# Kernel optimization log

Hardware: AMD Instinct MI355X
Metric: run time of the kernel (lower is better)

The kernel has to match this reference:

```python
import jax, jax.numpy as jnp
import numpy as np

B, N, H, HEADS = 8, 1024, 512, 4  # batch graphs, nodes/graph, graph_hsz, attention heads
R = 64  # relations per graph (passthrough)


def setup_inputs() -> dict:
    key = jax.random.key(0)
    k1, k2, k3, k4, k5, k6, k7 = jax.random.split(key, 7)
    adjs = jax.random.randint(k1, (B, N, N), 0, 2, dtype=jnp.int32)  # 0 => masked
    nodes = jax.random.normal(k2, (B, N, H), dtype=jnp.float32)
    triples = jax.random.normal(k3, (B, R, H), dtype=jnp.float32)   # unused in gat path
    relations = jax.random.normal(k4, (B, R, H), dtype=jnp.float32)  # passthrough
    node_num = jnp.full((B,), N, dtype=jnp.int32)  # all graphs full => no padding branch
    s = 1.0 / np.sqrt(H)
    Wq = (jax.random.normal(k5, (H, H), dtype=jnp.float32) * s)
    Wk = (jax.random.normal(k6, (H, H), dtype=jnp.float32) * s)
    Wv = (jax.random.normal(k7, (H, H), dtype=jnp.float32) * s)
    return {"adjs": adjs, "triples": triples, "nodes": nodes, "node_num": node_num,
            "relations": relations, "Wq": Wq, "Wk": Wk, "Wv": Wv}


def reference(adjs, triples, nodes, node_num, relations, Wq, Wk, Wv):
    b, n, h = nodes.shape
    dk = h // HEADS
    scale = 1.0 / jnp.sqrt(jnp.float32(h))  # torch divides by sqrt(key_dim)=sqrt(H)

    def to_heads(x, W):  # [B,N,H] -> [B,heads,N,dk]; matches split(dim=-1)+stack
        return (x @ W).reshape(b, n, HEADS, dk).transpose(0, 2, 1, 3)

    Q = to_heads(nodes, Wq)
    K = to_heads(nodes, Wk)
    V = to_heads(nodes, Wv)
    att = jnp.einsum('bhnd,bhmd->bhnm', Q, K) * scale
    att = jnp.where((adjs == 0)[:, None, :, :], -jnp.inf, att)
    p = jax.nn.softmax(att, axis=-1)  # dropout_p = blockdrop = 0.0 => identity
    out = jnp.einsum('bhnm,bhmd->bhnd', p, V)
    out = out.transpose(0, 2, 1, 3).reshape(b, n, h)  # concat heads along feature dim
    out = jax.nn.relu(out)
    return (out, relations)
```

## Files before the change

### kernel.cpp

```cpp
#include <hip/hip_runtime.h>
#include <stdint.h>

typedef __attribute__((ext_vector_type(4))) float f32x4;
typedef __attribute__((ext_vector_type(16))) float f32x16;
typedef __attribute__((ext_vector_type(8))) short bf16x8;
typedef unsigned long long ull;

#define GLB_AS const __attribute__((address_space(1)))
#define LDS_AS __attribute__((address_space(3)))

__device__ __forceinline__ short f2bf(float f) {
    union { float f; unsigned u; } x; x.f = f;
    unsigned r = x.u + 0x7FFFu + ((x.u >> 16) & 1u);
    return (short)(r >> 16);
}
__device__ __forceinline__ float bf2f(short s) {
    union { unsigned u; float f; } x; x.u = ((unsigned)(unsigned short)s) << 16;
    return x.f;
}

__global__ void k_pre(const float* __restrict__ nodes, short* __restrict__ nodes_bf,
                      const float* __restrict__ Wq, const float* __restrict__ Wk,
                      const float* __restrict__ Wv, short* __restrict__ WT,
                      const int* __restrict__ adjs, unsigned* __restrict__ packed) {
    int bi = blockIdx.x, tid = threadIdx.x;
    if (bi < 2048) {
        int i = (bi * 256 + tid) * 8;
        float4 a = *(const float4*)(nodes + i);
        float4 b = *(const float4*)(nodes + i + 4);
        bf16x8 v;
        v[0] = f2bf(a.x); v[1] = f2bf(a.y); v[2] = f2bf(a.z); v[3] = f2bf(a.w);
        v[4] = f2bf(b.x); v[5] = f2bf(b.y); v[6] = f2bf(b.z); v[7] = f2bf(b.w);
        *(bf16x8*)(nodes_bf + i) = v;
    } else if (bi < 5120) {
        int g = (bi - 2048) * 256 + tid;
        int j = g >> 9, k = g & 511;
        int w = j >> 9, n = j & 511;
        const float* W = (w == 0) ? Wq : (w == 1) ? Wk : Wv;
        WT[g] = f2bf(W[k * 512 + n]);
    } else {
        int g = (bi - 5120) * 256 + tid;
        int wv = g >> 6, lane = g & 63;
        ull m = __ballot(adjs[(size_t)wv * 64 + lane] != 0);
        if (lane == 0) *(ull*)(packed + (size_t)wv * 2) = m;
    }
}

__global__ __launch_bounds__(256) void k_gemm_qkv(const short* __restrict__ A,
                                                  const short* __restrict__ WT,
                                                  short* __restrict__ C) {
    __shared__ short Asm[2][128 * 32];
    __shared__ short Bsm[2][128 * 32];
    const int tid = threadIdx.x;
    const int l = tid & 63, w = tid >> 6;
    const int wr = w >> 1, wc = w & 1;
    const int c16 = l & 15, g = l >> 4;
    const int wg = blockIdx.x;
    const int swz = (wg & 7) * 96 + (wg >> 3);
    const int row0 = (swz / 12) * 128, n0 = (swz % 12) * 128;
    f32x4 acc[4][4] = {};

    auto stage = [&](int kt, int bsel) {
        const int k0 = kt * 32;
#pragma unroll
        for (int i = 0; i < 2; ++i) {
            int ch = tid + 256 * i;
            int r = ch >> 2, gc = ch & 3;
            __builtin_amdgcn_global_load_lds((GLB_AS unsigned*)(A + (row0 + r) * 512 + k0 + 8 * gc),
                                             (LDS_AS unsigned*)(&Asm[bsel][ch * 8]), 16, 0, 0);
            __builtin_amdgcn_global_load_lds((GLB_AS unsigned*)(WT + (n0 + r) * 512 + k0 + 8 * gc),
                                             (LDS_AS unsigned*)(&Bsm[bsel][ch * 8]), 16, 0, 0);
        }
    };

    stage(0, 0);
    asm volatile("s_waitcnt vmcnt(0)" ::: "memory");
    __syncthreads();

    for (int kt = 0; kt < 16; ++kt) {
        const int cur = kt & 1;
        if (kt < 15) stage(kt + 1, cur ^ 1);
        bf16x8 af[4], bfr[4];
#pragma unroll
        for (int mf = 0; mf < 4; ++mf)
            af[mf] = *(const bf16x8*)&Asm[cur][(wr * 64 + mf * 16 + c16) * 32 + 8 * g];
#pragma unroll
        for (int nf = 0; nf < 4; ++nf)
            bfr[nf] = *(const bf16x8*)&Bsm[cur][(wc * 64 + nf * 16 + c16) * 32 + 8 * g];
#pragma unroll
        for (int mf = 0; mf < 4; ++mf)
#pragma unroll
            for (int nf = 0; nf < 4; ++nf)
                acc[mf][nf] = __builtin_amdgcn_mfma_f32_16x16x32_bf16(af[mf], bfr[nf], acc[mf][nf], 0, 0, 0);
        asm volatile("s_waitcnt vmcnt(0)" ::: "memory");
        __syncthreads();
    }
#pragma unroll
    for (int mf = 0; mf < 4; ++mf)
#pragma unroll
        for (int nf = 0; nf < 4; ++nf) {
            const float cs = (n0 + wc * 64 + nf * 16 < 512) ? 0.06375872022286384f : 1.0f;
#pragma unroll
            for (int r = 0; r < 4; ++r) {
                int row = row0 + wr * 64 + mf * 16 + 4 * g + r;
                int col = n0 + wc * 64 + nf * 16 + c16;
                C[row * 1536 + col] = f2bf(acc[mf][nf][r] * cs);
            }
        }
}

__global__ __launch_bounds__(256) void k_mid(const short* __restrict__ QKV, short* __restrict__ Vt,
                                             const float* __restrict__ rel_in, float* __restrict__ rel_out) {
    __shared__ short tile[64 * 65];
    const int bi = blockIdx.x, t = threadIdx.x;
    if (bi >= 1024) {
        int i = ((bi - 1024) * 256 + t) * 4;
        *(float4*)(rel_out + i) = *(const float4*)(rel_in + i);
        return;
    }
    const int b = bi >> 7, n0 = ((bi >> 3) & 15) * 64, d0 = (bi & 7) * 64;
#pragma unroll
    for (int i = 0; i < 16; ++i) {
        int idx = t + 256 * i;
        int nn = idx >> 6, dd = idx & 63;
        tile[nn * 65 + dd] = QKV[(b * 1024 + n0 + nn) * 1536 + 1024 + d0 + dd];
    }
    __syncthreads();
#pragma unroll
    for (int i = 0; i < 16; ++i) {
        int idx = t + 256 * i;
        int dd = idx >> 6, nn = idx & 63;
        Vt[(b * 512 + d0 + dd) * 1024 + n0 + nn] = tile[nn * 65 + dd];
    }
}

__global__ __launch_bounds__(256, 2) void k_attn(const short* __restrict__ QKV, const short* __restrict__ Vt,
                                                 const unsigned* __restrict__ packed,
                                                 float* __restrict__ o0, short* __restrict__ o1,
                                                 float* __restrict__ lpart) {
    __shared__ short Ksm[2][64 * 128];
    __shared__ short Vsm[2][128 * 64];
    const int bh = blockIdx.x;
    const int b = bh >> 2, h = bh & 3;
    const int q0 = blockIdx.y * 128;
    const int mh = blockIdx.z;
    const int tid = threadIdx.x, l = tid & 63, wid = tid >> 6;
    const int l31 = l & 31, hi = l >> 5;
    const int qw = q0 + wid * 32;
    const int mbase = mh * 512;

    bf16x8 aq[8];
    const short* Qb = QKV + (size_t)(b * 1024 + qw + l31) * 1536 + h * 128;
#pragma unroll
    for (int kk = 0; kk < 8; ++kk)
        aq[kk] = *(const bf16x8*)(Qb + kk * 16 + hi * 8);

    f32x16 acc[4] = {};
    float l_lane = 0.f;

    const short* Kbase = QKV + (size_t)(b * 1024) * 1536 + 512 + h * 128;
    const short* Vtbase = Vt + (size_t)(b * 512 + h * 128) * 1024;
    const ull* adjq = (const ull*)packed + (size_t)(b * 1024 + qw + l31) * 16 + mh * 8;

    auto stage = [&](int t, int bsel) {
        const int m0 = mbase + t * 64;
#pragma unroll
        for (int i = 0; i < 4; ++i) {
            int ch = tid + 256 * i;
            int mr = ch >> 4, gc = ch & 15;
            int gs = gc ^ (mr & 15);
            __builtin_amdgcn_global_load_lds((GLB_AS unsigned*)(Kbase + (size_t)(m0 + mr) * 1536 + 8 * gs),
                                             (LDS_AS unsigned*)(&Ksm[bsel][ch * 8]), 16, 0, 0);
        }
#pragma unroll
        for (int i = 0; i < 4; ++i) {
            int ch = tid + 256 * i;
            int dr = ch >> 3, gc = ch & 7;
            int gs = gc ^ (dr & 7);
            __builtin_amdgcn_global_load_lds((GLB_AS unsigned*)(Vtbase + (size_t)dr * 1024 + m0 + 8 * gs),
                                             (LDS_AS unsigned*)(&Vsm[bsel][ch * 8]), 16, 0, 0);
        }
    };

    ull mcur = adjq[0], mnxt = 0;
    stage(0, 0);
    asm volatile("s_waitcnt vmcnt(0)" ::: "memory");
    __builtin_amdgcn_s_barrier();

    for (int t = 0; t < 8; ++t) {
        const int cur = t & 1;
        if (t < 7) {
            mnxt = adjq[t + 1];
            stage(t + 1, cur ^ 1);
        }

        f32x16 s[2] = {};
        __builtin_amdgcn_s_setprio(1);
#pragma unroll
        for (int kk = 0; kk < 8; ++kk)
#pragma unroll
            for (int mm = 0; mm < 2; ++mm) {
                const int row = mm * 32 + l31;
                const int chunk = (2 * kk + hi) ^ (row & 15);
                bf16x8 ak = *(const bf16x8*)&Ksm[cur][row * 128 + chunk * 8];
                s[mm] = __builtin_amdgcn_mfma_f32_32x32x16_bf16(ak, aq[kk], s[mm], 0, 0, 0);
            }
        __builtin_amdgcn_s_setprio(0);

        unsigned pk[2][4][2];
        float lt = 0.f;
#pragma unroll
        for (int mm = 0; mm < 2; ++mm) {
            const unsigned mshift = (unsigned)(mcur >> (32 * mm + 4 * hi));
#pragma unroll
            for (int j = 0; j < 4; ++j) {
                float p[4];
#pragma unroll
                for (int r = 0; r < 4; ++r) {
                    float e = __builtin_amdgcn_exp2f(s[mm][4 * j + r]);
                    p[r] = ((mshift >> (8 * j + r)) & 1u) ? e : 0.f;
                }
                lt += (p[0] + p[1]) + (p[2] + p[3]);
                asm("v_cvt_pk_bf16_f32 %0, %1, %2" : "=v"(pk[mm][j][0]) : "v"(p[0]), "v"(p[1]));
                asm("v_cvt_pk_bf16_f32 %0, %1, %2" : "=v"(pk[mm][j][1]) : "v"(p[2]), "v"(p[3]));
            }
        }
        l_lane += lt;

        union fragu { unsigned u[4]; bf16x8 v; };
        fragu frag[4];
#pragma unroll
        for (int mm = 0; mm < 2; ++mm)
#pragma unroll
            for (int kh = 0; kh < 2; ++kh) {
                unsigned a0 = pk[mm][2 * kh][0], a1 = pk[mm][2 * kh][1];
                unsigned b0 = pk[mm][2 * kh + 1][0], b1 = pk[mm][2 * kh + 1][1];
                unsigned rx0 = (unsigned)__shfl_xor((int)a0, 32);
                unsigned rx1 = (unsigned)__shfl_xor((int)a1, 32);
                unsigned rx2 = (unsigned)__shfl_xor((int)b0, 32);
                unsigned rx3 = (unsigned)__shfl_xor((int)b1, 32);
                fragu f;
                f.u[0] = hi ? rx2 : a0;
                f.u[1] = hi ? rx3 : a1;
                f.u[2] = hi ? b0 : rx0;
                f.u[3] = hi ? b1 : rx1;
                frag[2 * mm + kh] = f;
            }

        if (t < 7) { asm volatile("s_waitcnt vmcnt(9)" ::: "memory"); }
        else       { asm volatile("s_waitcnt vmcnt(0)" ::: "memory"); }
        __builtin_amdgcn_s_barrier();

        __builtin_amdgcn_s_setprio(1);
#pragma unroll
        for (int ks = 0; ks < 4; ++ks)
#pragma unroll
            for (int dd = 0; dd < 4; ++dd) {
                const int row = dd * 32 + l31;
                const int chunk = (2 * ks + hi) ^ (row & 7);
                bf16x8 bv = *(const bf16x8*)&Vsm[cur][row * 64 + chunk * 8];
                acc[dd] = __builtin_amdgcn_mfma_f32_32x32x16_bf16(frag[ks].v, bv, acc[dd], 0, 0, 0);
            }
        __builtin_amdgcn_s_setprio(0);

        mcur = mnxt;

        if (t < 7) {
            asm volatile("s_waitcnt vmcnt(4)" ::: "memory");
            __builtin_amdgcn_s_barrier();
        }
    }

    l_lane += __shfl_xor(l_lane, 32);

    if (mh == 0) {
#pragma unroll
        for (int dd = 0; dd < 4; ++dd)
#pragma unroll
            for (int j = 0; j < 4; ++j)
#pragma unroll
                for (int r = 0; r < 4; ++r) {
                    int q32 = r + 8 * j + 4 * hi;
                    o0[(size_t)(b * 1024 + qw + q32) * 512 + h * 128 + dd * 32 + l31] = acc[dd][4 * j + r];
                }
    } else {
#pragma unroll
        for (int dd = 0; dd < 4; ++dd)
#pragma unroll
            for (int j = 0; j < 4; ++j)
#pragma unroll
                for (int r = 0; r < 4; ++r) {
                    int q32 = r + 8 * j + 4 * hi;
                    o1[(size_t)(b * 1024 + qw + q32) * 512 + h * 128 + dd * 32 + l31] = f2bf(acc[dd][4 * j + r]);
                }
    }
    if (hi == 0)
        lpart[mh * 32768 + (b * 4 + h) * 1024 + qw + l31] = l_lane;
}

__global__ void k_combine(float* __restrict__ out, const short* __restrict__ o1,
                          const float* __restrict__ lp) {
    int i = (blockIdx.x * 256 + threadIdx.x) * 8;
    int b = i >> 19;
    int q = (i >> 9) & 1023;
    int h = (i >> 7) & 3;
    int lidx = (b * 4 + h) * 1024 + q;
    float inv = 1.f / (lp[lidx] + lp[32768 + lidx]);
    float4 a0 = *(const float4*)(out + i);
    float4 a1 = *(const float4*)(out + i + 4);
    bf16x8 c = *(const bf16x8*)(o1 + i);
    float4 r0, r1;
    r0.x = fmaxf((a0.x + bf2f(c[0])) * inv, 0.f);
    r0.y = fmaxf((a0.y + bf2f(c[1])) * inv, 0.f);
    r0.z = fmaxf((a0.z + bf2f(c[2])) * inv, 0.f);
    r0.w = fmaxf((a0.w + bf2f(c[3])) * inv, 0.f);
    r1.x = fmaxf((a1.x + bf2f(c[4])) * inv, 0.f);
    r1.y = fmaxf((a1.y + bf2f(c[5])) * inv, 0.f);
    r1.z = fmaxf((a1.z + bf2f(c[6])) * inv, 0.f);
    r1.w = fmaxf((a1.w + bf2f(c[7])) * inv, 0.f);
    *(float4*)(out + i) = r0;
    *(float4*)(out + i + 4) = r1;
}

extern "C" void kernel_launch(void* const* d_in, const int* in_sizes, int n_in,
                              void* d_out, int out_size, void* d_ws, size_t ws_size,
                              hipStream_t stream) {
    const int*   adjs      = (const int*)d_in[0];
    const float* nodes     = (const float*)d_in[2];
    const float* relations = (const float*)d_in[4];
    const float* Wq        = (const float*)d_in[5];
    const float* Wk        = (const float*)d_in[6];
    const float* Wv        = (const float*)d_in[7];

    char* ws = (char*)d_ws;
    short* nodes_bf   = (short*)(ws);
    short* WT         = (short*)(ws + 8388608);
    short* QKV        = (short*)(ws + 9961472);
    short* Vt         = (short*)(ws + 35127296);
    unsigned* adjpack = (unsigned*)(ws + 43515904);
    short* opart1 = (short*)(ws);
    float* lpart  = (float*)(ws + 8388608);

    float* out     = (float*)d_out;
    float* out_rel = out + 4194304;

    k_pre<<<dim3(37888), dim3(256), 0, stream>>>(nodes, nodes_bf, Wq, Wk, Wv, WT, adjs, adjpack);
    k_gemm_qkv<<<dim3(768), dim3(256), 0, stream>>>(nodes_bf, WT, QKV);
    k_mid<<<dim3(1280), dim3(256), 0, stream>>>(QKV, Vt, relations, out_rel);
    k_attn<<<dim3(32, 8, 2), dim3(256), 0, stream>>>(QKV, Vt, adjpack, out, opart1, lpart);
    k_combine<<<dim3(2048), dim3(256), 0, stream>>>(out, opart1, lpart);
}
```

Baseline: 84.72 us.

## Software-pipeline QK of next tile against softmax+PV of previous tile

Restructures the attention loop so the QK^T MFMAs for tile t run alongside the exp/mask/PV work for tile t-1. V gets triple buffering in LDS and the intermediate scores are double-buffered in registers. Each iteration now has a single barrier instead of two. The aim is to hide softmax ALU latency and barrier stalls behind matrix work, at the cost of more LDS (which may hurt occupancy at 2 blocks/CU) and more VGPRs for sreg.

```diff
diff --git a/kernel.cpp b/kernel.cpp
--- a/kernel.cpp
+++ b/kernel.cpp
@@ -139,7 +139,7 @@
                                                  float* __restrict__ o0, short* __restrict__ o1,
                                                  float* __restrict__ lpart) {
     __shared__ short Ksm[2][64 * 128];
-    __shared__ short Vsm[2][128 * 64];
+    __shared__ short Vsm[3][128 * 64];
     const int bh = blockIdx.x;
     const int b = bh >> 2, h = bh & 3;
     const int q0 = blockIdx.y * 128;
@@ -156,13 +156,14 @@
         aq[kk] = *(const bf16x8*)(Qb + kk * 16 + hi * 8);
 
     f32x16 acc[4] = {};
+    f32x16 sreg[2][2];
     float l_lane = 0.f;
 
     const short* Kbase = QKV + (size_t)(b * 1024) * 1536 + 512 + h * 128;
     const short* Vtbase = Vt + (size_t)(b * 512 + h * 128) * 1024;
     const ull* adjq = (const ull*)packed + (size_t)(b * 1024 + qw + l31) * 16 + mh * 8;
 
-    auto stage = [&](int t, int bsel) {
+    auto stageK = [&](int t, int kb) {
         const int m0 = mbase + t * 64;
 #pragma unroll
         for (int i = 0; i < 4; ++i) {
@@ -170,31 +171,23 @@
             int mr = ch >> 4, gc = ch & 15;
             int gs = gc ^ (mr & 15);
             __builtin_amdgcn_global_load_lds((GLB_AS unsigned*)(Kbase + (size_t)(m0 + mr) * 1536 + 8 * gs),
-                                             (LDS_AS unsigned*)(&Ksm[bsel][ch * 8]), 16, 0, 0);
-        }
+                                             (LDS_AS unsigned*)(&Ksm[kb][ch * 8]), 16, 0, 0);
+        }
+    };
+    auto stageV = [&](int t, int vb) {
+        const int m0 = mbase + t * 64;
 #pragma unroll
         for (int i = 0; i < 4; ++i) {
             int ch = tid + 256 * i;
             int dr = ch >> 3, gc = ch & 7;
             int gs = gc ^ (dr & 7);
             __builtin_amdgcn_global_load_lds((GLB_AS unsigned*)(Vtbase + (size_t)dr * 1024 + m0 + 8 * gs),
-                                             (LDS_AS unsigned*)(&Vsm[bsel][ch * 8]), 16, 0, 0);
-        }
-    };
-
-    ull mcur = adjq[0], mnxt = 0;
-    stage(0, 0);
-    asm volatile("s_waitcnt vmcnt(0)" ::: "memory");
-    __builtin_amdgcn_s_barrier();
-
-    for (int t = 0; t < 8; ++t) {
-        const int cur = t & 1;
-        if (t < 7) {
-            mnxt = adjq[t + 1];
-            stage(t + 1, cur ^ 1);
-        }
-
-        f32x16 s[2] = {};
+                                             (LDS_AS unsigned*)(&Vsm[vb][ch * 8]), 16, 0, 0);
+        }
+    };
+
+    auto QK = [&](int kb, f32x16* sd) {
+        sd[0] = (f32x16)0.f; sd[1] = (f32x16)0.f;
         __builtin_amdgcn_s_setprio(1);
 #pragma unroll
         for (int kk = 0; kk < 8; ++kk)
@@ -202,39 +195,37 @@
             for (int mm = 0; mm < 2; ++mm) {
                 const int row = mm * 32 + l31;
                 const int chunk = (2 * kk + hi) ^ (row & 15);
-                bf16x8 ak = *(const bf16x8*)&Ksm[cur][row * 128 + chunk * 8];
-                s[mm] = __builtin_amdgcn_mfma_f32_32x32x16_bf16(ak, aq[kk], s[mm], 0, 0, 0);
+                bf16x8 ak = *(const bf16x8*)&Ksm[kb][row * 128 + chunk * 8];
+                sd[mm] = __builtin_amdgcn_mfma_f32_32x32x16_bf16(ak, aq[kk], sd[mm], 0, 0, 0);
             }
         __builtin_amdgcn_s_setprio(0);
-
-        unsigned pk[2][4][2];
+    };
+
+    union fragu { unsigned u[4]; bf16x8 v; };
+
+    auto SMAXPV = [&](const f32x16* sv, ull msk, int vb) {
+        fragu frag[4];
         float lt = 0.f;
 #pragma unroll
         for (int mm = 0; mm < 2; ++mm) {
-            const unsigned mshift = (unsigned)(mcur >> (32 * mm + 4 * hi));
+            const unsigned mshift = (unsigned)(msk >> (32 * mm + 4 * hi));
+            unsigned pk[4][2];
 #pragma unroll
             for (int j = 0; j < 4; ++j) {
                 float p[4];
 #pragma unroll
                 for (int r = 0; r < 4; ++r) {
-                    float e = __builtin_amdgcn_exp2f(s[mm][4 * j + r]);
+                    float e = __builtin_amdgcn_exp2f(sv[mm][4 * j + r]);
                     p[r] = ((mshift >> (8 * j + r)) & 1u) ? e : 0.f;
                 }
                 lt += (p[0] + p[1]) + (p[2] + p[3]);
-                asm("v_cvt_pk_bf16_f32 %0, %1, %2" : "=v"(pk[mm][j][0]) : "v"(p[0]), "v"(p[1]));
-                asm("v_cvt_pk_bf16_f32 %0, %1, %2" : "=v"(pk[mm][j][1]) : "v"(p[2]), "v"(p[3]));
-            }
-        }
-        l_lane += lt;
-
-        union fragu { unsigned u[4]; bf16x8 v; };
-        fragu frag[4];
-#pragma unroll
-        for (int mm = 0; mm < 2; ++mm)
+                asm("v_cvt_pk_bf16_f32 %0, %1, %2" : "=v"(pk[j][0]) : "v"(p[0]), "v"(p[1]));
+                asm("v_cvt_pk_bf16_f32 %0, %1, %2" : "=v"(pk[j][1]) : "v"(p[2]), "v"(p[3]));
+            }
 #pragma unroll
             for (int kh = 0; kh < 2; ++kh) {
-                unsigned a0 = pk[mm][2 * kh][0], a1 = pk[mm][2 * kh][1];
-                unsigned b0 = pk[mm][2 * kh + 1][0], b1 = pk[mm][2 * kh + 1][1];
+                unsigned a0 = pk[2 * kh][0], a1 = pk[2 * kh][1];
+                unsigned b0 = pk[2 * kh + 1][0], b1 = pk[2 * kh + 1][1];
                 unsigned rx0 = (unsigned)__shfl_xor((int)a0, 32);
                 unsigned rx1 = (unsigned)__shfl_xor((int)a1, 32);
                 unsigned rx2 = (unsigned)__shfl_xor((int)b0, 32);
@@ -246,11 +237,8 @@
                 f.u[3] = hi ? b1 : rx1;
                 frag[2 * mm + kh] = f;
             }
-
-        if (t < 7) { asm volatile("s_waitcnt vmcnt(9)" ::: "memory"); }
-        else       { asm volatile("s_waitcnt vmcnt(0)" ::: "memory"); }
-        __builtin_amdgcn_s_barrier();
-
+        }
+        l_lane += lt;
         __builtin_amdgcn_s_setprio(1);
 #pragma unroll
         for (int ks = 0; ks < 4; ++ks)
@@ -258,18 +246,38 @@
             for (int dd = 0; dd < 4; ++dd) {
                 const int row = dd * 32 + l31;
                 const int chunk = (2 * ks + hi) ^ (row & 7);
-                bf16x8 bv = *(const bf16x8*)&Vsm[cur][row * 64 + chunk * 8];
+                bf16x8 bv = *(const bf16x8*)&Vsm[vb][row * 64 + chunk * 8];
                 acc[dd] = __builtin_amdgcn_mfma_f32_32x32x16_bf16(frag[ks].v, bv, acc[dd], 0, 0, 0);
             }
         __builtin_amdgcn_s_setprio(0);
-
-        mcur = mnxt;
-
+    };
+
+    ull mPrev = adjq[0], mCur, mNext = 0;
+    stageK(0, 0); stageV(0, 0);
+    asm volatile("s_waitcnt vmcnt(0)" ::: "memory");
+    __builtin_amdgcn_s_barrier();
+    QK(0, sreg[0]);
+    mCur = adjq[1];
+    stageK(1, 1); stageV(1, 1);
+    asm volatile("s_waitcnt vmcnt(4)" ::: "memory");
+    __builtin_amdgcn_s_barrier();
+
+#pragma unroll
+    for (int t = 1; t < 8; ++t) {
+        const int kb = t & 1;
+        QK(kb, sreg[kb]);
         if (t < 7) {
-            asm volatile("s_waitcnt vmcnt(4)" ::: "memory");
-            __builtin_amdgcn_s_barrier();
-        }
-    }
+            mNext = adjq[t + 1];
+            stageK(t + 1, kb ^ 1);
+            stageV(t + 1, (t + 1) % 3);
+        }
+        SMAXPV(sreg[kb ^ 1], mPrev, (t - 1) % 3);
+        mPrev = mCur; mCur = mNext;
+        if (t < 7) { asm volatile("s_waitcnt vmcnt(4)" ::: "memory"); }
+        else       { asm volatile("s_waitcnt vmcnt(0)" ::: "memory"); }
+        __builtin_amdgcn_s_barrier();
+    }
+    SMAXPV(sreg[1], mPrev, 7 % 3);
 
     l_lane += __shfl_xor(l_lane, 32);
 
```

Result: faster. 82.74 us (-2.3%).

## Split attention key range four ways with smaller tiles and higher occupancy

Applied to the files above, without the earlier changes.

The attention kernel now splits the 1024 keys into four chunks of 256 instead of two of 512. It also halves the per-iteration key tile to 32 rows, which shrinks LDS use and allows three blocks per CU. All four partial outputs are written as bf16 to a separate workspace region, and the combine kernel sums four partials and four softmax denominators. This raises the grid from 512 to 1024 blocks to fill the GPU better. The cost is extra partial-output traffic and bf16 rounding of every partial, where before one partial stayed in fp32.

```diff
diff --git a/kernel.cpp b/kernel.cpp
--- a/kernel.cpp
+++ b/kernel.cpp
@@ -134,12 +134,11 @@
     }
 }
 
-__global__ __launch_bounds__(256, 2) void k_attn(const short* __restrict__ QKV, const short* __restrict__ Vt,
+__global__ __launch_bounds__(256, 3) void k_attn(const short* __restrict__ QKV, const short* __restrict__ Vt,
                                                  const unsigned* __restrict__ packed,
-                                                 float* __restrict__ o0, short* __restrict__ o1,
-                                                 float* __restrict__ lpart) {
-    __shared__ short Ksm[2][64 * 128];
-    __shared__ short Vsm[2][128 * 64];
+                                                 short* __restrict__ opart, float* __restrict__ lpart) {
+    __shared__ short Ksm[2][32 * 128];
+    __shared__ short Vsm[2][128 * 32];
     const int bh = blockIdx.x;
     const int b = bh >> 2, h = bh & 3;
     const int q0 = blockIdx.y * 128;
@@ -147,7 +146,7 @@
     const int tid = threadIdx.x, l = tid & 63, wid = tid >> 6;
     const int l31 = l & 31, hi = l >> 5;
     const int qw = q0 + wid * 32;
-    const int mbase = mh * 512;
+    const int mbase = mh * 256;
 
     bf16x8 aq[8];
     const short* Qb = QKV + (size_t)(b * 1024 + qw + l31) * 1536 + h * 128;
@@ -160,12 +159,12 @@
 
     const short* Kbase = QKV + (size_t)(b * 1024) * 1536 + 512 + h * 128;
     const short* Vtbase = Vt + (size_t)(b * 512 + h * 128) * 1024;
-    const ull* adjq = (const ull*)packed + (size_t)(b * 1024 + qw + l31) * 16 + mh * 8;
+    const unsigned* adjw = packed + (size_t)(b * 1024 + qw + l31) * 32 + mh * 8;
 
     auto stage = [&](int t, int bsel) {
-        const int m0 = mbase + t * 64;
-#pragma unroll
-        for (int i = 0; i < 4; ++i) {
+        const int m0 = mbase + t * 32;
+#pragma unroll
+        for (int i = 0; i < 2; ++i) {
             int ch = tid + 256 * i;
             int mr = ch >> 4, gc = ch & 15;
             int gs = gc ^ (mr & 15);
@@ -173,92 +172,86 @@
                                              (LDS_AS unsigned*)(&Ksm[bsel][ch * 8]), 16, 0, 0);
         }
 #pragma unroll
-        for (int i = 0; i < 4; ++i) {
+        for (int i = 0; i < 2; ++i) {
             int ch = tid + 256 * i;
-            int dr = ch >> 3, gc = ch & 7;
-            int gs = gc ^ (dr & 7);
+            int dr = ch >> 2, gc = ch & 3;
+            int gs = gc ^ (dr & 3);
             __builtin_amdgcn_global_load_lds((GLB_AS unsigned*)(Vtbase + (size_t)dr * 1024 + m0 + 8 * gs),
                                              (LDS_AS unsigned*)(&Vsm[bsel][ch * 8]), 16, 0, 0);
         }
     };
 
-    ull mcur = adjq[0], mnxt = 0;
+    unsigned mcur = adjw[0], mnxt = 0;
     stage(0, 0);
     asm volatile("s_waitcnt vmcnt(0)" ::: "memory");
     __builtin_amdgcn_s_barrier();
 
+#pragma unroll
     for (int t = 0; t < 8; ++t) {
         const int cur = t & 1;
         if (t < 7) {
-            mnxt = adjq[t + 1];
+            mnxt = adjw[t + 1];
             stage(t + 1, cur ^ 1);
         }
 
-        f32x16 s[2] = {};
+        f32x16 s = (f32x16)0.f;
         __builtin_amdgcn_s_setprio(1);
 #pragma unroll
-        for (int kk = 0; kk < 8; ++kk)
-#pragma unroll
-            for (int mm = 0; mm < 2; ++mm) {
-                const int row = mm * 32 + l31;
-                const int chunk = (2 * kk + hi) ^ (row & 15);
-                bf16x8 ak = *(const bf16x8*)&Ksm[cur][row * 128 + chunk * 8];
-                s[mm] = __builtin_amdgcn_mfma_f32_32x32x16_bf16(ak, aq[kk], s[mm], 0, 0, 0);
+        for (int kk = 0; kk < 8; ++kk) {
+            const int row = l31;
+            const int chunk = (2 * kk + hi) ^ (row & 15);
+            bf16x8 ak = *(const bf16x8*)&Ksm[cur][row * 128 + chunk * 8];
+            s = __builtin_amdgcn_mfma_f32_32x32x16_bf16(ak, aq[kk], s, 0, 0, 0);
+        }
+        __builtin_amdgcn_s_setprio(0);
+
+        unsigned pk[4][2];
+        const unsigned mshift = mcur >> (4 * hi);
+        float lt = 0.f;
+#pragma unroll
+        for (int j = 0; j < 4; ++j) {
+            float p[4];
+#pragma unroll
+            for (int r = 0; r < 4; ++r) {
+                float e = __builtin_amdgcn_exp2f(s[4 * j + r]);
+                p[r] = ((mshift >> (8 * j + r)) & 1u) ? e : 0.f;
             }
-        __builtin_amdgcn_s_setprio(0);
-
-        unsigned pk[2][4][2];
-        float lt = 0.f;
-#pragma unroll
-        for (int mm = 0; mm < 2; ++mm) {
-            const unsigned mshift = (unsigned)(mcur >> (32 * mm + 4 * hi));
-#pragma unroll
-            for (int j = 0; j < 4; ++j) {
-                float p[4];
-#pragma unroll
-                for (int r = 0; r < 4; ++r) {
-                    float e = __builtin_amdgcn_exp2f(s[mm][4 * j + r]);
-                    p[r] = ((mshift >> (8 * j + r)) & 1u) ? e : 0.f;
-                }
-                lt += (p[0] + p[1]) + (p[2] + p[3]);
-                asm("v_cvt_pk_bf16_f32 %0, %1, %2" : "=v"(pk[mm][j][0]) : "v"(p[0]), "v"(p[1]));
-                asm("v_cvt_pk_bf16_f32 %0, %1, %2" : "=v"(pk[mm][j][1]) : "v"(p[2]), "v"(p[3]));
-            }
+            lt += (p[0] + p[1]) + (p[2] + p[3]);
+            asm("v_cvt_pk_bf16_f32 %0, %1, %2" : "=v"(pk[j][0]) : "v"(p[0]), "v"(p[1]));
+            asm("v_cvt_pk_bf16_f32 %0, %1, %2" : "=v"(pk[j][1]) : "v"(p[2]), "v"(p[3]));
         }
         l_lane += lt;
 
         union fragu { unsigned u[4]; bf16x8 v; };
-        fragu frag[4];
-#pragma unroll
-        for (int mm = 0; mm < 2; ++mm)
-#pragma unroll
-            for (int kh = 0; kh < 2; ++kh) {
-                unsigned a0 = pk[mm][2 * kh][0], a1 = pk[mm][2 * kh][1];
-                unsigned b0 = pk[mm][2 * kh + 1][0], b1 = pk[mm][2 * kh + 1][1];
-                unsigned rx0 = (unsigned)__shfl_xor((int)a0, 32);
-                unsigned rx1 = (unsigned)__shfl_xor((int)a1, 32);
-                unsigned rx2 = (unsigned)__shfl_xor((int)b0, 32);
-                unsigned rx3 = (unsigned)__shfl_xor((int)b1, 32);
-                fragu f;
-                f.u[0] = hi ? rx2 : a0;
-                f.u[1] = hi ? rx3 : a1;
-                f.u[2] = hi ? b0 : rx0;
-                f.u[3] = hi ? b1 : rx1;
-                frag[2 * mm + kh] = f;
-            }
-
-        if (t < 7) { asm volatile("s_waitcnt vmcnt(9)" ::: "memory"); }
+        fragu frag[2];
+#pragma unroll
+        for (int kh = 0; kh < 2; ++kh) {
+            unsigned a0 = pk[2 * kh][0], a1 = pk[2 * kh][1];
+            unsigned b0 = pk[2 * kh + 1][0], b1 = pk[2 * kh + 1][1];
+            unsigned rx0 = (unsigned)__shfl_xor((int)a0, 32);
+            unsigned rx1 = (unsigned)__shfl_xor((int)a1, 32);
+            unsigned rx2 = (unsigned)__shfl_xor((int)b0, 32);
+            unsigned rx3 = (unsigned)__shfl_xor((int)b1, 32);
+            fragu f;
+            f.u[0] = hi ? rx2 : a0;
+            f.u[1] = hi ? rx3 : a1;
+            f.u[2] = hi ? b0 : rx0;
+            f.u[3] = hi ? b1 : rx1;
+            frag[kh] = f;
+        }
+
+        if (t < 7) { asm volatile("s_waitcnt vmcnt(5)" ::: "memory"); }
         else       { asm volatile("s_waitcnt vmcnt(0)" ::: "memory"); }
         __builtin_amdgcn_s_barrier();
 
         __builtin_amdgcn_s_setprio(1);
 #pragma unroll
-        for (int ks = 0; ks < 4; ++ks)
+        for (int ks = 0; ks < 2; ++ks)
 #pragma unroll
             for (int dd = 0; dd < 4; ++dd) {
                 const int row = dd * 32 + l31;
-                const int chunk = (2 * ks + hi) ^ (row & 7);
-                bf16x8 bv = *(const bf16x8*)&Vsm[cur][row * 64 + chunk * 8];
+                const int chunk = (2 * ks + hi) ^ (row & 3);
+                bf16x8 bv = *(const bf16x8*)&Vsm[cur][row * 32 + chunk * 8];
                 acc[dd] = __builtin_amdgcn_mfma_f32_32x32x16_bf16(frag[ks].v, bv, acc[dd], 0, 0, 0);
             }
         __builtin_amdgcn_s_setprio(0);
@@ -266,58 +259,48 @@
         mcur = mnxt;
 
         if (t < 7) {
-            asm volatile("s_waitcnt vmcnt(4)" ::: "memory");
+            asm volatile("s_waitcnt vmcnt(2)" ::: "memory");
             __builtin_amdgcn_s_barrier();
         }
     }
 
     l_lane += __shfl_xor(l_lane, 32);
 
-    if (mh == 0) {
-#pragma unroll
-        for (int dd = 0; dd < 4; ++dd)
-#pragma unroll
-            for (int j = 0; j < 4; ++j)
-#pragma unroll
-                for (int r = 0; r < 4; ++r) {
-                    int q32 = r + 8 * j + 4 * hi;
-                    o0[(size_t)(b * 1024 + qw + q32) * 512 + h * 128 + dd * 32 + l31] = acc[dd][4 * j + r];
-                }
-    } else {
-#pragma unroll
-        for (int dd = 0; dd < 4; ++dd)
-#pragma unroll
-            for (int j = 0; j < 4; ++j)
-#pragma unroll
-                for (int r = 0; r < 4; ++r) {
-                    int q32 = r + 8 * j + 4 * hi;
-                    o1[(size_t)(b * 1024 + qw + q32) * 512 + h * 128 + dd * 32 + l31] = f2bf(acc[dd][4 * j + r]);
-                }
-    }
+#pragma unroll
+    for (int dd = 0; dd < 4; ++dd)
+#pragma unroll
+        for (int j = 0; j < 4; ++j)
+#pragma unroll
+            for (int r = 0; r < 4; ++r) {
+                int q32 = r + 8 * j + 4 * hi;
+                opart[(size_t)mh * 4194304 + (size_t)(b * 1024 + qw + q32) * 512 + h * 128 + dd * 32 + l31]
+                    = f2bf(acc[dd][4 * j + r]);
+            }
     if (hi == 0)
         lpart[mh * 32768 + (b * 4 + h) * 1024 + qw + l31] = l_lane;
 }
 
-__global__ void k_combine(float* __restrict__ out, const short* __restrict__ o1,
+__global__ void k_combine(float* __restrict__ out, const short* __restrict__ op,
                           const float* __restrict__ lp) {
     int i = (blockIdx.x * 256 + threadIdx.x) * 8;
     int b = i >> 19;
     int q = (i >> 9) & 1023;
     int h = (i >> 7) & 3;
     int lidx = (b * 4 + h) * 1024 + q;
-    float inv = 1.f / (lp[lidx] + lp[32768 + lidx]);
-    float4 a0 = *(const float4*)(out + i);
-    float4 a1 = *(const float4*)(out + i + 4);
-    bf16x8 c = *(const bf16x8*)(o1 + i);
+    float inv = 1.f / (lp[lidx] + lp[32768 + lidx] + lp[65536 + lidx] + lp[98304 + lidx]);
+    bf16x8 c0 = *(const bf16x8*)(op + i);
+    bf16x8 c1 = *(const bf16x8*)(op + 4194304 + i);
+    bf16x8 c2 = *(const bf16x8*)(op + 8388608 + i);
+    bf16x8 c3 = *(const bf16x8*)(op + 12582912 + i);
     float4 r0, r1;
-    r0.x = fmaxf((a0.x + bf2f(c[0])) * inv, 0.f);
-    r0.y = fmaxf((a0.y + bf2f(c[1])) * inv, 0.f);
-    r0.z = fmaxf((a0.z + bf2f(c[2])) * inv, 0.f);
-    r0.w = fmaxf((a0.w + bf2f(c[3])) * inv, 0.f);
-    r1.x = fmaxf((a1.x + bf2f(c[4])) * inv, 0.f);
-    r1.y = fmaxf((a1.y + bf2f(c[5])) * inv, 0.f);
-    r1.z = fmaxf((a1.z + bf2f(c[6])) * inv, 0.f);
-    r1.w = fmaxf((a1.w + bf2f(c[7])) * inv, 0.f);
+    r0.x = fmaxf((bf2f(c0[0]) + bf2f(c1[0]) + bf2f(c2[0]) + bf2f(c3[0])) * inv, 0.f);
+    r0.y = fmaxf((bf2f(c0[1]) + bf2f(c1[1]) + bf2f(c2[1]) + bf2f(c3[1])) * inv, 0.f);
+    r0.z = fmaxf((bf2f(c0[2]) + bf2f(c1[2]) + bf2f(c2[2]) + bf2f(c3[2])) * inv, 0.f);
+    r0.w = fmaxf((bf2f(c0[3]) + bf2f(c1[3]) + bf2f(c2[3]) + bf2f(c3[3])) * inv, 0.f);
+    r1.x = fmaxf((bf2f(c0[4]) + bf2f(c1[4]) + bf2f(c2[4]) + bf2f(c3[4])) * inv, 0.f);
+    r1.y = fmaxf((bf2f(c0[5]) + bf2f(c1[5]) + bf2f(c2[5]) + bf2f(c3[5])) * inv, 0.f);
+    r1.z = fmaxf((bf2f(c0[6]) + bf2f(c1[6]) + bf2f(c2[6]) + bf2f(c3[6])) * inv, 0.f);
+    r1.w = fmaxf((bf2f(c0[7]) + bf2f(c1[7]) + bf2f(c2[7]) + bf2f(c3[7])) * inv, 0.f);
     *(float4*)(out + i) = r0;
     *(float4*)(out + i + 4) = r1;
 }
@@ -338,8 +321,8 @@
     short* QKV        = (short*)(ws + 9961472);
     short* Vt         = (short*)(ws + 35127296);
     unsigned* adjpack = (unsigned*)(ws + 43515904);
-    short* opart1 = (short*)(ws);
-    float* lpart  = (float*)(ws + 8388608);
+    short* opart      = (short*)(ws + 44564480);
+    float* lpart      = (float*)(ws + 8388608);
 
     float* out     = (float*)d_out;
     float* out_rel = out + 4194304;
@@ -347,6 +330,6 @@
     k_pre<<<dim3(37888), dim3(256), 0, stream>>>(nodes, nodes_bf, Wq, Wk, Wv, WT, adjs, adjpack);
     k_gemm_qkv<<<dim3(768), dim3(256), 0, stream>>>(nodes_bf, WT, QKV);
     k_mid<<<dim3(1280), dim3(256), 0, stream>>>(QKV, Vt, relations, out_rel);
-    k_attn<<<dim3(32, 8, 2), dim3(256), 0, stream>>>(QKV, Vt, adjpack, out, opart1, lpart);
-    k_combine<<<dim3(2048), dim3(256), 0, stream>>>(out, opart1, lpart);
-}
+    k_attn<<<dim3(32, 8, 4), dim3(256), 0, stream>>>(QKV, Vt, adjpack, opart, lpart);
+    k_combine<<<dim3(2048), dim3(256), 0, stream>>>(out, opart, lpart);
+}
```

Result: slower. 91.94 us (+8.5%).
